# Performance work log

Hardware: AMD Instinct MI355X
Metric: run time of the kernel (lower is better)

## Reference

```python
import jax, jax.numpy as jnp
import numpy as np

B, C, H = 4, 256, 8
GRID = 64                  # 64x64 quads, 2 triangles each
F = 2 * GRID * GRID        # 8192 faces
D = C // H
N_STEPS = 4 * GRID + 8     # upper bound on BFS wavefronts over the face graph


def _grid_adjacency():
    """Face adjacency (<=3 neighbors, -1 padded) of a triangulated GRIDxGRID quad grid."""
    adj = -np.ones((F, 3), np.int32)
    qid = lambda r, c: 2 * (r * GRID + c)
    for r in range(GRID):
        for c in range(GRID):
            t0 = qid(r, c); t1 = t0 + 1
            n0, n1 = [t1], [t0]
            if c > 0:        n0.append(qid(r, c - 1) + 1)
            if r > 0:        n0.append(qid(r - 1, c) + 1)
            if c < GRID - 1: n1.append(qid(r, c + 1))
            if r < GRID - 1: n1.append(qid(r + 1, c))
            adj[t0, :len(n0)] = n0
            adj[t1, :len(n1)] = n1
    return adj


def setup_inputs() -> dict:
    key = jax.random.key(0)
    k1, k2, k3, k4 = jax.random.split(key, 4)
    x = jax.random.normal(k1, (B, C, F), jnp.float32)
    Wq = jax.random.normal(k2, (C, C), jnp.float32) / np.sqrt(C).astype(np.float32)
    Wk = jax.random.normal(k3, (C, C), jnp.float32) / np.sqrt(C).astype(np.float32)
    adj = jnp.tile(jnp.asarray(_grid_adjacency())[None], (B, 1, 1))
    anchors = jax.random.randint(k4, (B,), 0, F, jnp.int32)
    return {"x": x, "Wq": Wq, "Wk": Wk, "adj": adj, "anchors": anchors}


def _heads(W, x):
    """Project and L2-normalize per head: [B,C,F] -> [B,H,D,F] unit vectors along D."""
    y = jnp.einsum('oc,bcf->bof', W, x).reshape(x.shape[0], H, D, -1)
    return y * jax.lax.rsqrt(jnp.sum(y * y, axis=2, keepdims=True) + 1e-12)


def reference(x, Wq, Wk, adj, anchors):
    q = _heads(Wq, x)          # [B,H,D,F]
    k = _heads(Wk, x)          # [B,H,D,F]
    bidx = jnp.arange(B)

    # initial scores: normalized attention map between all faces and the anchor face,
    # mapped to [0,1] and averaged over heads  (atnmap+1)/2 path of the torch module
    k_anchor = k[bidx, :, :, anchors]                       # [B,H,D]
    cos0 = jnp.einsum('bhdf,bhd->bhf', q, k_anchor)         # [B,H,F]
    scores0 = (jnp.mean(cos0, axis=1) + 1.0) * 0.5          # [B,F]

    ktot = k.sum(axis=3)                                    # [B,H,D]
    valid = adj >= 0
    adj_s = jnp.where(valid, adj, 0)
    done0 = jnp.zeros((B, F), bool).at[bidx, anchors].set(True)
    boundary0 = done0

    def gather(v):  # v: [B,F] -> neighbor values [B,F,3]
        return jnp.take_along_axis(v, adj_s.reshape(B, -1), axis=1).reshape(B, F, 3)

    def step(carry, _):
        done, boundary, scores = carry
        bf = boundary.astype(x.dtype)
        nb = bf.sum(1)                       # |boundary|
        no = F - nb                          # |others| = complement of boundary
        # mean over (heads, boundary, others) of cosine(q_b, k_o):
        # mean_{b,o} q_b.k_o = (sum_b q_b).(sum_o k_o) / (nb*no)
        qs = jnp.einsum('bhdf,bf->bhd', q, bf)
        ko = ktot - jnp.einsum('bhdf,bf->bhd', k, bf)
        mean_cos = jnp.einsum('bhd,bhd->b', qs, ko) / (H * jnp.maximum(nb * no, 1.0))
        pred = (mean_cos + 1.0) * 0.5        # scalar per mesh, as in torch reshape(1,-1).mean
        # neighbor score: max score among already-visited (done) adjacent faces, else 1
        n_done = gather(done) & valid
        n_sc = gather(scores)
        neigh = jnp.where(jnp.any(n_done, -1),
                          jnp.max(jnp.where(n_done, n_sc, -jnp.inf), -1), 1.0)
        cand = jnp.minimum(jnp.maximum(pred[:, None], scores), neigh)
        scores = jnp.where(boundary, cand, scores)
        done = done | boundary
        boundary = jnp.any(gather(boundary) & valid, -1) & ~done
        return (done, boundary, scores), None

    (_, _, scores), _ = jax.lax.scan(jax.checkpoint(step),
                                     (done0, boundary0, scores0), None, length=N_STEPS)
    # with atn_layers=1 the torch module never modifies features: final_features == x
    return x, scores
```

## Files before the change

kernel.cpp:

```cpp
#include <hip/hip_runtime.h>
#include <hip/hip_bf16.h>
#include <stdint.h>

#define B_ 4
#define C_ 256
#define H_ 8
#define F_ 8192
#define NSTEPS_ 264
#define OC_ 512

typedef __attribute__((ext_vector_type(8))) short short8;
typedef __attribute__((ext_vector_type(4))) float f32x4;

static __device__ __forceinline__ unsigned f2bf(float f) {
  unsigned u = __float_as_uint(f);
  return (u + 0x7FFFu + ((u >> 16) & 1u)) >> 16;
}
static __device__ __forceinline__ float b2f(unsigned short s) {
  return __uint_as_float(((unsigned)s) << 16);
}

static __device__ __forceinline__ void face_neighbors(int f, int nn[3]) {
  int qd = f >> 1, r = qd >> 6, c = qd & 63;
  if ((f & 1) == 0) {
    nn[0] = f + 1;
    nn[1] = (c > 0) ? f - 1 : -1;
    nn[2] = (r > 0) ? f - 127 : -1;
  } else {
    nn[0] = f - 1;
    nn[1] = (c < 63) ? f + 1 : -1;
    nn[2] = (r < 63) ? f + 127 : -1;
  }
}

static __device__ __forceinline__ int face_dist(int ra, int ca, int pa, int f) {
  int qd = f >> 1, r = qd >> 6, c = qd & 63, p = f & 1;
  int dr = r - ra, dc = c - ca;
  int I = max(dr, 0) + max(dc, 0);
  int D = max(-dr, 0) + max(-dc, 0);
  int lo = pa ? max(2 * I - 1, 2 * D) : max(2 * I, 2 * D - 1);
  lo = max(lo, 0);
  lo += (lo ^ p ^ pa) & 1;
  return lo;
}

__global__ void k_pre(const float* __restrict__ Wq, const float* __restrict__ Wk,
                      uint16_t* __restrict__ Wbf) {
  const int gid = blockIdx.x * 256 + threadIdx.x;
  const int base = gid * 32;
  const float* src = (base < 65536) ? (Wq + base) : (Wk + (base - 65536));
  uint32_t pk[16];
#pragma unroll
  for (int j = 0; j < 16; ++j) {
    float2 v = *(const float2*)(src + j * 2);
    pk[j] = f2bf(v.x) | (f2bf(v.y) << 16);
  }
  uint4* dst = (uint4*)(Wbf + base);
#pragma unroll
  for (int s = 0; s < 4; ++s)
    dst[s] = make_uint4(pk[4 * s], pk[4 * s + 1], pk[4 * s + 2], pk[4 * s + 3]);
}

__launch_bounds__(256)
__global__ void k_gemm(const float* __restrict__ x, const uint16_t* __restrict__ Wbf,
                       uint16_t* __restrict__ qkT, const int* __restrict__ anchors,
                       uint16_t* __restrict__ order_g, uint32_t* __restrict__ lvlOff_g,
                       uint32_t* __restrict__ chunks_g, uint32_t* __restrict__ nch_g,
                       float* __restrict__ ktot) {
  __shared__ char smem[49152];
  char* Xl = smem;
  char* Wl = smem + 32768;
  const int tid = threadIdx.x;
  const int b = blockIdx.z;

  if (blockIdx.x == 128) {
    uint8_t* dLv = (uint8_t*)smem;
    uint16_t* ordL = (uint16_t*)(smem + 8192);
    uint32_t* hist = (uint32_t*)(smem + 24576);
    uint32_t* loff = (uint32_t*)(smem + 25600);
    uint32_t* cnt = (uint32_t*)(smem + 26640);
    uint32_t* chOff = (uint32_t*)(smem + 27680);
    const int a = anchors[b];
    const int aq = a >> 1, ra = aq >> 6, ca = aq & 63, pa = a & 1;
    hist[tid] = 0; cnt[tid] = 0;
    __syncthreads();
#pragma unroll
    for (int j = 0; j < 32; ++j) {
      int f = j * 256 + tid;
      int d = face_dist(ra, ca, pa, f);
      dLv[f] = (uint8_t)d;
      atomicAdd(&hist[d], 1u);
    }
    __syncthreads();
    loff[tid + 1] = hist[tid];
    if (tid == 0) loff[0] = 0;
    __syncthreads();
    for (int ofs = 1; ofs < 256; ofs <<= 1) {
      uint32_t v = (tid >= ofs) ? loff[tid + 1 - ofs] : 0u;
      __syncthreads();
      loff[tid + 1] += v;
      __syncthreads();
    }
#pragma unroll
    for (int j = 0; j < 32; ++j) {
      int f = j * 256 + tid;
      int d = dLv[f];
      int nn[3];
      face_neighbors(f, nn);
      int mask = 0;
      if (nn[0] >= 0 && dLv[nn[0]] < d) mask |= 1;
      if (nn[1] >= 0 && dLv[nn[1]] < d) mask |= 2;
      if (nn[2] >= 0 && dLv[nn[2]] < d) mask |= 4;
      uint32_t pos = loff[d] + atomicAdd(&cnt[d], 1u);
      ordL[pos] = (uint16_t)(f | (mask << 13));
    }
    __syncthreads();
    for (int i = tid; i < F_; i += 256) order_g[b * F_ + i] = ordL[i];
    for (int l = tid; l < NSTEPS_ + 2; l += 256)
      lvlOff_g[b * (NSTEPS_ + 2) + l] = (l <= 256) ? loff[l] : (uint32_t)F_;
    const int n_l = (int)(loff[tid + 1] - loff[tid]);
    const int chc = (n_l + 63) >> 6;
    chOff[tid + 1] = (uint32_t)chc;
    if (tid == 0) chOff[0] = 0;
    __syncthreads();
    for (int ofs = 1; ofs < 256; ofs <<= 1) {
      uint32_t v = (tid >= ofs) ? chOff[tid + 1 - ofs] : 0u;
      __syncthreads();
      chOff[tid + 1] += v;
      __syncthreads();
    }
    const uint32_t cbase = chOff[tid];
    for (int j = 0; j < chc; ++j) {
      uint32_t cs = loff[tid] + (uint32_t)(j * 64);
      uint32_t cl = (uint32_t)min(64, n_l - j * 64);
      chunks_g[b * 512 + cbase + j] = cs | (cl << 16);
    }
    if (tid == 255) nch_g[b] = chOff[256];
    return;
  }

  const int f0 = blockIdx.x * 64;
  const int lane = tid & 63;
  const int wo = tid >> 6;
  const int lq = lane >> 4;
  const int lm = lane & 15;

  {
    const int fx = tid & 63;
    const int kseg = tid >> 6;
    const float* src = x + ((size_t)b * C_ + kseg * 64) * F_ + f0 + fx;
#pragma unroll
    for (int g = 0; g < 4; ++g) {
      uint32_t pk[8];
#pragma unroll
      for (int j2 = 0; j2 < 8; ++j2) {
        float v0 = src[(size_t)(g * 16 + 2 * j2) * F_];
        float v1 = src[(size_t)(g * 16 + 2 * j2 + 1) * F_];
        pk[j2] = f2bf(v0) | (f2bf(v1) << 16);
      }
#pragma unroll
      for (int s = 0; s < 2; ++s) {
        int slot = kseg * 8 + g * 2 + s;
        uint32_t* dst = (uint32_t*)(Xl + (size_t)fx * 512 + ((slot ^ (fx & 7)) << 4));
        dst[0] = pk[4 * s + 0]; dst[1] = pk[4 * s + 1];
        dst[2] = pk[4 * s + 2]; dst[3] = pk[4 * s + 3];
      }
    }
  }

  for (int p = 0; p < 4; ++p) {
    const int o0 = p * 128;
    const uint16_t* Wsrc = Wbf + (size_t)o0 * C_;
    f32x4 acc[4][2] = {};
    for (int kt = 0; kt < 4; ++kt) {
      __syncthreads();
#pragma unroll
      for (int j = 0; j < 4; ++j) {
        int sl = tid * 4 + j;
        int ocl = sl >> 3, slot = sl & 7;
        uint4 v = *(const uint4*)(Wsrc + (size_t)ocl * C_ + kt * 64 + slot * 8);
        *(uint4*)(Wl + (size_t)ocl * 128 + ((slot ^ (ocl & 7)) << 4)) = v;
      }
      __syncthreads();
#pragma unroll
      for (int kk = 0; kk < 64; kk += 32) {
        const int sA = kt * 8 + (kk >> 3) + lq;
        const int sB = (kk >> 3) + lq;
        short8 af[4], bg[2];
#pragma unroll
        for (int mi = 0; mi < 4; ++mi) {
          int fl = mi * 16 + lm;
          af[mi] = *(const short8*)(Xl + (size_t)fl * 512 + ((sA ^ (fl & 7)) << 4));
        }
#pragma unroll
        for (int ni = 0; ni < 2; ++ni) {
          int ocl = wo * 32 + ni * 16 + lm;
          bg[ni] = *(const short8*)(Wl + (size_t)ocl * 128 + ((sB ^ (ocl & 7)) << 4));
        }
#pragma unroll
        for (int mi = 0; mi < 4; ++mi)
#pragma unroll
          for (int ni = 0; ni < 2; ++ni)
            acc[mi][ni] = __builtin_amdgcn_mfma_f32_16x16x32_bf16(af[mi], bg[ni], acc[mi][ni], 0, 0, 0);
      }
    }
    __syncthreads();

    char* yst = Wl;
#pragma unroll
    for (int mi = 0; mi < 4; ++mi) {
#pragma unroll
      for (int r = 0; r < 4; ++r) {
        float s0 = acc[mi][0][r] * acc[mi][0][r] + acc[mi][1][r] * acc[mi][1][r];
        s0 += __shfl_xor(s0, 1);
        s0 += __shfl_xor(s0, 2);
        s0 += __shfl_xor(s0, 4);
        s0 += __shfl_xor(s0, 8);
        const float sc0 = rsqrtf(s0 + 1e-12f);
        const int fl = mi * 16 + lq * 4 + r;
#pragma unroll
        for (int ni = 0; ni < 2; ++ni) {
          int ocl = wo * 32 + ni * 16 + lm;
          float v = acc[mi][ni][r] * sc0;
          int byte = fl * 256 + ((((ocl * 2) >> 4) ^ (fl & 7)) << 4) + ((ocl * 2) & 15);
          *(uint16_t*)(yst + byte) = (uint16_t)f2bf(v);
        }
      }
    }
    __syncthreads();
    uint32_t* qk32 = (uint32_t*)qkT;
    const size_t obase = (((size_t)b * F_ + f0) * OC_ + o0) >> 1;
    for (int idx = tid; idx < 4096; idx += 256) {
      int face = idx >> 6, wd = idx & 63;
      int byte = face * 256 + ((((wd * 4) >> 4) ^ (face & 7)) << 4) + ((wd * 4) & 15);
      qk32[obase + (size_t)face * 256 + wd] = *(uint32_t*)(yst + byte);
    }
    if (p >= 2 && tid < 128) {
      const int cbyte = tid * 2;
      float ssum = 0.f;
#pragma unroll 4
      for (int face = 0; face < 64; ++face) {
        int byte = face * 256 + (((cbyte >> 4) ^ (face & 7)) << 4) + (cbyte & 15);
        ssum += b2f(*(const uint16_t*)(yst + byte));
      }
      atomicAdd(&ktot[b * C_ + (p - 2) * 128 + tid], ssum);
    }
  }
}

__launch_bounds__(256)
__global__ void k_predscore(const uint16_t* __restrict__ qkT, const uint16_t* __restrict__ order_g,
                            const uint32_t* __restrict__ lvlOff_g, const float* __restrict__ ktot,
                            const int* __restrict__ anchors, float* __restrict__ pred_g,
                            float* __restrict__ scores0) {
  const int b = blockIdx.y, tid = threadIdx.x, bx = blockIdx.x;
  __shared__ uint16_t ordS[384];
  __shared__ float qk2[512];
  __shared__ float red[256];
  if (bx >= NSTEPS_) {
    const int anchor = anchors[b];
    red[tid] = b2f(qkT[((size_t)(b * F_ + anchor)) * OC_ + 256 + tid]);
    __syncthreads();
    const int wave = tid >> 6, lane = tid & 63;
    const int fbase = (bx - NSTEPS_) * 256 + wave * 64;
    for (int fi = 0; fi < 64; ++fi) {
      int f = fbase + fi;
      const uint16_t* row = qkT + ((size_t)(b * F_ + f)) * OC_ + lane * 4;
      ushort4 rv = *(const ushort4*)row;
      float dot = b2f(rv.x) * red[lane * 4 + 0] + b2f(rv.y) * red[lane * 4 + 1] +
                  b2f(rv.z) * red[lane * 4 + 2] + b2f(rv.w) * red[lane * 4 + 3];
      for (int off = 32; off; off >>= 1) dot += __shfl_down(dot, off);
      if (lane == 0) scores0[b * F_ + f] = (dot * (1.0f / H_) + 1.f) * 0.5f;
    }
    return;
  }
  const int t = bx;
  const uint32_t s = lvlOff_g[b * (NSTEPS_ + 2) + t];
  const uint32_t e = lvlOff_g[b * (NSTEPS_ + 2) + t + 1];
  const int n = min((int)(e - s), 384);
  for (int i = tid; i < n; i += 256) ordS[i] = order_g[(size_t)b * F_ + s + i] & 8191;
  __syncthreads();
  const int half = tid >> 7, cc = (tid & 127) * 2;
  const uint16_t* qkb = qkT + ((size_t)b * F_) * OC_ + half * 256 + cc;
  float a0 = 0.f, a1 = 0.f;
  int i = 0;
  for (; i + 8 <= n; i += 8) {
    uint32_t v[8];
#pragma unroll
    for (int u = 0; u < 8; ++u) v[u] = *(const uint32_t*)(qkb + (size_t)ordS[i + u] * OC_);
#pragma unroll
    for (int u = 0; u < 8; ++u) {
      a0 += b2f((unsigned short)(v[u] & 0xFFFFu));
      a1 += b2f((unsigned short)(v[u] >> 16));
    }
  }
  for (; i < n; ++i) {
    uint32_t v = *(const uint32_t*)(qkb + (size_t)ordS[i] * OC_);
    a0 += b2f((unsigned short)(v & 0xFFFFu));
    a1 += b2f((unsigned short)(v >> 16));
  }
  qk2[half * 256 + cc] = a0;
  qk2[half * 256 + cc + 1] = a1;
  __syncthreads();
  float prod = qk2[tid] * (ktot[b * C_ + tid] - qk2[256 + tid]);
  red[tid] = prod;
  __syncthreads();
  if (tid < 128) red[tid] += red[tid + 128];
  __syncthreads();
  if (tid < 64) {
    float v = red[tid] + red[tid + 64];
    for (int off = 32; off; off >>= 1) v += __shfl_down(v, off);
    if (tid == 0) {
      float nb = (float)(e - s), no = (float)F_ - nb;
      pred_g[b * NSTEPS_ + t] = (v / ((float)H_ * fmaxf(nb * no, 1.f)) + 1.f) * 0.5f;
    }
  }
}

#define MKST(ENT, ACT, I0, I1, I2, IO, IW, M)            \
  do {                                                   \
    int f_ = (int)((ENT) & 8191u);                       \
    int m_ = (int)(((ENT) >> 13) & 7u);                  \
    int s_ = 1 - 2 * (f_ & 1);                           \
    I0 = (m_ & 1) ? f_ + s_ : f_;                        \
    I1 = (m_ & 2) ? f_ - s_ : f_;                        \
    I2 = (m_ & 4) ? f_ - 127 * s_ : f_;                  \
    IO = f_;                                             \
    IW = (ACT) ? f_ : (F_ + lane);                       \
    M = m_;                                              \
  } while (0)

__launch_bounds__(256)
__global__ void k_final(const float* __restrict__ scores0, const uint16_t* __restrict__ order_g,
                        const uint32_t* __restrict__ chunks_g, const uint32_t* __restrict__ nch_g,
                        const float* __restrict__ pred_g, const int* __restrict__ anchors,
                        const float4* __restrict__ x4, float4* __restrict__ out4,
                        float* __restrict__ out_scores) {
  __shared__ float A[F_ + 64];
  __shared__ uint16_t ordL[F_];
  __shared__ float prL[NSTEPS_];
  __shared__ uint32_t chunkL[512];
  __shared__ int nchS;
  const int tid = threadIdx.x;
  if (blockIdx.x >= B_) {
    const int cb = blockIdx.x - B_;
    const float4* src = x4 + (size_t)cb * 16384 + tid;
    float4* dst = out4 + (size_t)cb * 16384 + tid;
#pragma unroll 8
    for (int it = 0; it < 64; ++it) dst[it * 256] = src[it * 256];
    return;
  }
  const int b = blockIdx.x;
  for (int i = tid; i < NSTEPS_; i += 256) prL[i] = pred_g[b * NSTEPS_ + i];
  for (int i = tid; i < 512; i += 256) chunkL[i] = chunks_g[b * 512 + i];
  if (tid == 0) nchS = (int)nch_g[b];
  const int a = anchors[b];
  const int aq = a >> 1, ra = aq >> 6, ca = aq & 63, pa = a & 1;
  __syncthreads();
  for (int i = tid; i < F_; i += 256) {
    int d = face_dist(ra, ca, pa, i);
    A[i] = fmaxf(prL[d], scores0[(size_t)b * F_ + i]);
  }
  for (int i = tid; i < F_ / 4; i += 256)
    ((ushort4*)ordL)[i] = ((const ushort4*)(order_g + (size_t)b * F_))[i];
  __syncthreads();
  if (tid < 64) {
    const int lane = tid;
    const int nch = nchS;
    int i0a = 0, i1a = 0, i2a = 0, ioa = 0, iwa = F_ + lane, ma = 0;
    int i0b = 0, i1b = 0, i2b = 0, iob = 0, iwb = F_ + lane, mb = 0;
    {
      uint32_t ck = chunkL[0];
      uint32_t bs = ck & 0xFFFFu, cn = ck >> 16;
      uint32_t ent = ordL[bs + min((uint32_t)lane, cn - 1)];
      MKST(ent, (uint32_t)lane < cn, i0a, i1a, i2a, ioa, iwa, ma);
    }
    if (nch > 1) {
      uint32_t ck = chunkL[1];
      uint32_t bs = ck & 0xFFFFu, cn = ck >> 16;
      uint32_t ent = ordL[bs + min((uint32_t)lane, cn - 1)];
      MKST(ent, (uint32_t)lane < cn, i0b, i1b, i2b, iob, iwb, mb);
    }
    uint32_t ckN = (nch > 2) ? chunkL[2] : 0;
    for (int c = 0; c < nch; ++c) {
      float v0 = A[i0a], v1 = A[i1a], v2 = A[i2a], own = A[ioa];
      uint32_t entN = 0;
      bool actN = false;
      if (c + 2 < nch) {
        uint32_t bs = ckN & 0xFFFFu, cn = ckN >> 16;
        entN = ordL[bs + min((uint32_t)lane, cn - 1)];
        actN = (uint32_t)lane < cn;
      }
      uint32_t ckNN = (c + 3 < nch) ? chunkL[c + 3] : 0;
      float m0 = (ma & 1) ? v0 : -1e30f;
      float m1 = (ma & 2) ? v1 : -1e30f;
      float m2 = (ma & 4) ? v2 : -1e30f;
      float nv = ma ? fmaxf(fmaxf(m0, m1), m2) : 1.0f;
      A[iwa] = fminf(own, nv);
      i0a = i0b; i1a = i1b; i2a = i2b; ioa = iob; iwa = iwb; ma = mb;
      MKST(entN, actN, i0b, i1b, i2b, iob, iwb, mb);
      ckN = ckNN;
    }
  }
  __syncthreads();
  for (int i = tid; i < F_ / 4; i += 256)
    ((float4*)(out_scores + (size_t)b * F_))[i] = ((const float4*)A)[i];
}

extern "C" void kernel_launch(void* const* d_in, const int* in_sizes, int n_in,
                              void* d_out, int out_size, void* d_ws, size_t ws_size,
                              hipStream_t stream) {
  const float* x = (const float*)d_in[0];
  const float* Wq = (const float*)d_in[1];
  const float* Wk = (const float*)d_in[2];
  const int* anchors = (const int*)d_in[4];
  float* out = (float*)d_out;

  uint16_t* qkT = (uint16_t*)d_out;

  char* ws = (char*)d_ws;
  size_t off = 0;
  uint16_t* Wbf = (uint16_t*)(ws + off);   off += (size_t)OC_ * C_ * 2;
  float* ktot = (float*)(ws + off);        off += (size_t)B_ * C_ * 4;
  float* scores0 = (float*)(ws + off);     off += (size_t)B_ * F_ * 4;
  float* pred = (float*)(ws + off);        off += (size_t)B_ * NSTEPS_ * 4;
  uint16_t* order = (uint16_t*)(ws + off); off += (size_t)B_ * F_ * 2;
  uint32_t* lvlOff = (uint32_t*)(ws + off); off += (size_t)B_ * (NSTEPS_ + 2) * 4;
  uint32_t* chunks = (uint32_t*)(ws + off); off += (size_t)B_ * 512 * 4;
  uint32_t* nch = (uint32_t*)(ws + off);   off += (size_t)B_ * 4;

  k_pre<<<16, 256, 0, stream>>>(Wq, Wk, Wbf);
  hipMemsetAsync(ktot, 0, (size_t)B_ * C_ * 4, stream);
  k_gemm<<<dim3(129, 1, B_), 256, 0, stream>>>(x, Wbf, qkT, anchors, order, lvlOff,
                                               chunks, nch, ktot);
  k_predscore<<<dim3(NSTEPS_ + 32, B_), 256, 0, stream>>>(qkT, order, lvlOff, ktot, anchors,
                                                          pred, scores0);
  k_final<<<B_ + 128, 256, 0, stream>>>(scores0, order, chunks, nch, pred, anchors,
                                        (const float4*)x, (float4*)out,
                                        out + (size_t)B_ * C_ * F_);
}
```

Baseline: 145.9 us.

## Process BFS levels in pairs to halve the serial wavefront chain

Chunks now cover two consecutive BFS levels at once. Each face in the odd-parity half resolves its predecessors' values inline by looking two hops back, using a per-face predecessor mask stored in LDS. This roughly halves the number of serialized single-wave chunk iterations in the final scan. In exchange each lane does more LDS gathers, carries more registers and needs an extra mask array. Correctness depends on the parity reasoning holding for every anchor position.

Result: slower. 157.0 us (+7.6%).

```diff
diff --git a/kernel.cpp b/kernel.cpp
--- a/kernel.cpp
+++ b/kernel.cpp
@@ -66,7 +66,7 @@
                        uint16_t* __restrict__ qkT, const int* __restrict__ anchors,
                        uint16_t* __restrict__ order_g, uint32_t* __restrict__ lvlOff_g,
                        uint32_t* __restrict__ chunks_g, uint32_t* __restrict__ nch_g,
-                       float* __restrict__ ktot) {
+                       uint8_t* __restrict__ maskF_g, float* __restrict__ ktot) {
   __shared__ char smem[49152];
   char* Xl = smem;
   char* Wl = smem + 32768;
@@ -113,14 +113,21 @@
       if (nn[2] >= 0 && dLv[nn[2]] < d) mask |= 4;
       uint32_t pos = loff[d] + atomicAdd(&cnt[d], 1u);
       ordL[pos] = (uint16_t)(f | (mask << 13));
+      maskF_g[(size_t)b * F_ + f] = (uint8_t)mask;
     }
     __syncthreads();
     for (int i = tid; i < F_; i += 256) order_g[b * F_ + i] = ordL[i];
     for (int l = tid; l < NSTEPS_ + 2; l += 256)
       lvlOff_g[b * (NSTEPS_ + 2) + l] = (l <= 256) ? loff[l] : (uint32_t)F_;
-    const int n_l = (int)(loff[tid + 1] - loff[tid]);
-    const int chc = (n_l + 63) >> 6;
-    chOff[tid + 1] = (uint32_t)chc;
+    uint32_t pbase = 0, pcnt = 0, chc = 0;
+    if (tid < 128) {
+      int l1 = 2 * tid + 1;
+      pbase = loff[l1];
+      uint32_t pend = loff[min(l1 + 2, 256)];
+      pcnt = pend - pbase;
+      chc = (pcnt + 63) >> 6;
+    }
+    chOff[tid + 1] = chc;
     if (tid == 0) chOff[0] = 0;
     __syncthreads();
     for (int ofs = 1; ofs < 256; ofs <<= 1) {
@@ -130,9 +137,9 @@
       __syncthreads();
     }
     const uint32_t cbase = chOff[tid];
-    for (int j = 0; j < chc; ++j) {
-      uint32_t cs = loff[tid] + (uint32_t)(j * 64);
-      uint32_t cl = (uint32_t)min(64, n_l - j * 64);
+    for (uint32_t j = 0; j < chc; ++j) {
+      uint32_t cs = pbase + j * 64;
+      uint32_t cl = min(64u, pcnt - j * 64);
       chunks_g[b * 512 + cbase + j] = cs | (cl << 16);
     }
     if (tid == 255) nch_g[b] = chOff[256];
@@ -317,27 +324,61 @@
   }
 }
 
-#define MKST(ENT, ACT, I0, I1, I2, IO, IW, M)            \
-  do {                                                   \
-    int f_ = (int)((ENT) & 8191u);                       \
-    int m_ = (int)(((ENT) >> 13) & 7u);                  \
-    int s_ = 1 - 2 * (f_ & 1);                           \
-    I0 = (m_ & 1) ? f_ + s_ : f_;                        \
-    I1 = (m_ & 2) ? f_ - s_ : f_;                        \
-    I2 = (m_ & 4) ? f_ - 127 * s_ : f_;                  \
-    IO = f_;                                             \
-    IW = (ACT) ? f_ : (F_ + lane);                       \
-    M = m_;                                              \
-  } while (0)
+
+#define SWPREP(SUF, CK, VALIDN)                                                  \
+  {                                                                              \
+    uint32_t bs_ = (CK) & 0xFFFFu, cn_ = (CK) >> 16;                             \
+    uint32_t ent_ = ordL[bs_ + min((uint32_t)lane, cn_ - 1u)];                   \
+    int f_ = (int)(ent_ & 8191u), s_ = 1 - 2 * (f_ & 1);                         \
+    m##SUF = (int)((ent_ >> 13) & 7u);                                           \
+    r2##SUF = ((f_ ^ pa) & 1) == 0;                                              \
+    p0##SUF = (m##SUF & 1) ? f_ + s_ : f_;                                       \
+    p1##SUF = (m##SUF & 2) ? f_ - s_ : f_;                                       \
+    p2##SUF = (m##SUF & 4) ? f_ - 127 * s_ : f_;                                 \
+    q00##SUF = (p0##SUF - s_) & 8191; q01##SUF = (p0##SUF + s_) & 8191;          \
+    q02##SUF = (p0##SUF + 127 * s_) & 8191;                                      \
+    q10##SUF = (p1##SUF - s_) & 8191; q11##SUF = (p1##SUF + s_) & 8191;          \
+    q12##SUF = (p1##SUF + 127 * s_) & 8191;                                      \
+    q20##SUF = (p2##SUF - s_) & 8191; q21##SUF = (p2##SUF + s_) & 8191;          \
+    q22##SUF = (p2##SUF + 127 * s_) & 8191;                                      \
+    io##SUF = f_;                                                                \
+    iw##SUF = ((VALIDN) && (uint32_t)lane < cn_) ? f_ : (F_ + lane);             \
+    mp0##SUF = mFL[p0##SUF]; mp1##SUF = mFL[p1##SUF]; mp2##SUF = mFL[p2##SUF];   \
+  }
+
+#define SWITER(SUF, NSUF, CK, VALIDN)                                            \
+  {                                                                              \
+    float rp0_ = A[p0##SUF], rp1_ = A[p1##SUF], rp2_ = A[p2##SUF];               \
+    float r00_ = A[q00##SUF], r01_ = A[q01##SUF], r02_ = A[q02##SUF];            \
+    float r10_ = A[q10##SUF], r11_ = A[q11##SUF], r12_ = A[q12##SUF];            \
+    float r20_ = A[q20##SUF], r21_ = A[q21##SUF], r22_ = A[q22##SUF];            \
+    float own_ = A[io##SUF];                                                     \
+    SWPREP(NSUF, CK, VALIDN);                                                    \
+    const float NI_ = -1e30f;                                                    \
+    float qm0_ = fmaxf(fmaxf((mp0##SUF & 1) ? r00_ : NI_, (mp0##SUF & 2) ? r01_ : NI_), \
+                       (mp0##SUF & 4) ? r02_ : NI_);                             \
+    float qm1_ = fmaxf(fmaxf((mp1##SUF & 1) ? r10_ : NI_, (mp1##SUF & 2) ? r11_ : NI_), \
+                       (mp1##SUF & 4) ? r12_ : NI_);                             \
+    float qm2_ = fmaxf(fmaxf((mp2##SUF & 1) ? r20_ : NI_, (mp2##SUF & 2) ? r21_ : NI_), \
+                       (mp2##SUF & 4) ? r22_ : NI_);                             \
+    float pm0_ = r2##SUF ? fminf(rp0_, qm0_) : rp0_;                             \
+    float pm1_ = r2##SUF ? fminf(rp1_, qm1_) : rp1_;                             \
+    float pm2_ = r2##SUF ? fminf(rp2_, qm2_) : rp2_;                             \
+    float nv_ = fmaxf(fmaxf((m##SUF & 1) ? pm0_ : NI_, (m##SUF & 2) ? pm1_ : NI_), \
+                      (m##SUF & 4) ? pm2_ : NI_);                                \
+    nv_ = m##SUF ? nv_ : 1.0f;                                                   \
+    A[iw##SUF] = fminf(own_, nv_);                                               \
+  }
 
 __launch_bounds__(256)
 __global__ void k_final(const float* __restrict__ scores0, const uint16_t* __restrict__ order_g,
                         const uint32_t* __restrict__ chunks_g, const uint32_t* __restrict__ nch_g,
                         const float* __restrict__ pred_g, const int* __restrict__ anchors,
-                        const float4* __restrict__ x4, float4* __restrict__ out4,
-                        float* __restrict__ out_scores) {
+                        const uint8_t* __restrict__ maskF_g, const float4* __restrict__ x4,
+                        float4* __restrict__ out4, float* __restrict__ out_scores) {
   __shared__ float A[F_ + 64];
   __shared__ uint16_t ordL[F_];
+  __shared__ uint8_t mFL[F_];
   __shared__ float prL[NSTEPS_];
   __shared__ uint32_t chunkL[512];
   __shared__ int nchS;
@@ -354,6 +395,8 @@
   for (int i = tid; i < NSTEPS_; i += 256) prL[i] = pred_g[b * NSTEPS_ + i];
   for (int i = tid; i < 512; i += 256) chunkL[i] = chunks_g[b * 512 + i];
   if (tid == 0) nchS = (int)nch_g[b];
+  for (int i = tid; i < F_ / 4; i += 256)
+    ((uint32_t*)mFL)[i] = ((const uint32_t*)(maskF_g + (size_t)b * F_))[i];
   const int a = anchors[b];
   const int aq = a >> 1, ra = aq >> 6, ca = aq & 63, pa = a & 1;
   __syncthreads();
@@ -367,39 +410,23 @@
   if (tid < 64) {
     const int lane = tid;
     const int nch = nchS;
-    int i0a = 0, i1a = 0, i2a = 0, ioa = 0, iwa = F_ + lane, ma = 0;
-    int i0b = 0, i1b = 0, i2b = 0, iob = 0, iwb = F_ + lane, mb = 0;
-    {
-      uint32_t ck = chunkL[0];
-      uint32_t bs = ck & 0xFFFFu, cn = ck >> 16;
-      uint32_t ent = ordL[bs + min((uint32_t)lane, cn - 1)];
-      MKST(ent, (uint32_t)lane < cn, i0a, i1a, i2a, ioa, iwa, ma);
-    }
-    if (nch > 1) {
-      uint32_t ck = chunkL[1];
-      uint32_t bs = ck & 0xFFFFu, cn = ck >> 16;
-      uint32_t ent = ordL[bs + min((uint32_t)lane, cn - 1)];
-      MKST(ent, (uint32_t)lane < cn, i0b, i1b, i2b, iob, iwb, mb);
-    }
+    int p0X, p1X, p2X, q00X, q01X, q02X, q10X, q11X, q12X, q20X, q21X, q22X;
+    int ioX, iwX, mX, mp0X, mp1X, mp2X; bool r2X;
+    int p0Y, p1Y, p2Y, q00Y, q01Y, q02Y, q10Y, q11Y, q12Y, q20Y, q21Y, q22Y;
+    int ioY, iwY, mY, mp0Y, mp1Y, mp2Y; bool r2Y;
+    uint32_t ck0 = (nch > 0) ? chunkL[0] : 0;
+    SWPREP(X, ck0, nch > 0);
+    uint32_t ckCur = (nch > 1) ? chunkL[1] : 0;
     uint32_t ckN = (nch > 2) ? chunkL[2] : 0;
-    for (int c = 0; c < nch; ++c) {
-      float v0 = A[i0a], v1 = A[i1a], v2 = A[i2a], own = A[ioa];
-      uint32_t entN = 0;
-      bool actN = false;
-      if (c + 2 < nch) {
-        uint32_t bs = ckN & 0xFFFFu, cn = ckN >> 16;
-        entN = ordL[bs + min((uint32_t)lane, cn - 1)];
-        actN = (uint32_t)lane < cn;
-      }
-      uint32_t ckNN = (c + 3 < nch) ? chunkL[c + 3] : 0;
-      float m0 = (ma & 1) ? v0 : -1e30f;
-      float m1 = (ma & 2) ? v1 : -1e30f;
-      float m2 = (ma & 4) ? v2 : -1e30f;
-      float nv = ma ? fmaxf(fmaxf(m0, m1), m2) : 1.0f;
-      A[iwa] = fminf(own, nv);
-      i0a = i0b; i1a = i1b; i2a = i2b; ioa = iob; iwa = iwb; ma = mb;
-      MKST(entN, actN, i0b, i1b, i2b, iob, iwb, mb);
-      ckN = ckNN;
+    int c = 0;
+    while (c < nch) {
+      SWITER(X, Y, ckCur, c + 1 < nch);
+      { uint32_t t_ = (c + 3 < nch) ? chunkL[c + 3] : 0; ckCur = ckN; ckN = t_; }
+      ++c;
+      if (c >= nch) break;
+      SWITER(Y, X, ckCur, c + 1 < nch);
+      { uint32_t t_ = (c + 3 < nch) ? chunkL[c + 3] : 0; ckCur = ckN; ckN = t_; }
+      ++c;
     }
   }
   __syncthreads();
@@ -428,14 +455,15 @@
   uint32_t* lvlOff = (uint32_t*)(ws + off); off += (size_t)B_ * (NSTEPS_ + 2) * 4;
   uint32_t* chunks = (uint32_t*)(ws + off); off += (size_t)B_ * 512 * 4;
   uint32_t* nch = (uint32_t*)(ws + off);   off += (size_t)B_ * 4;
+  uint8_t* maskF = (uint8_t*)(ws + off);   off += (size_t)B_ * F_;
 
   k_pre<<<16, 256, 0, stream>>>(Wq, Wk, Wbf);
   hipMemsetAsync(ktot, 0, (size_t)B_ * C_ * 4, stream);
   k_gemm<<<dim3(129, 1, B_), 256, 0, stream>>>(x, Wbf, qkT, anchors, order, lvlOff,
-                                               chunks, nch, ktot);
+                                               chunks, nch, maskF, ktot);
   k_predscore<<<dim3(NSTEPS_ + 32, B_), 256, 0, stream>>>(qkT, order, lvlOff, ktot, anchors,
                                                           pred, scores0);
-  k_final<<<B_ + 128, 256, 0, stream>>>(scores0, order, chunks, nch, pred, anchors,
+  k_final<<<B_ + 128, 256, 0, stream>>>(scores0, order, chunks, nch, pred, anchors, maskF,
                                         (const float4*)x, (float4*)out,
                                         out + (size_t)B_ * C_ * F_);
 }
```
